# Kernel tuning notes

Hardware: AMD Instinct MI355X
Metric: run time of the kernel (lower is better)

Reference implementation:

```python
import jax, jax.numpy as jnp
import numpy as np

SLOPE = 25.0  # fast-sigmoid surrogate slope (snntorch default)

@jax.custom_vjp
def spike(u):
    # Heaviside spike with fast-sigmoid surrogate gradient
    return (u > 0).astype(u.dtype)

def _spike_fwd(u):
    return spike(u), u

def _spike_bwd(u, g):
    return (g / (1.0 + SLOPE * jnp.abs(u)) ** 2,)

spike.defvjp(_spike_fwd, _spike_bwd)


def setup_inputs() -> dict:
    key = jax.random.key(0)
    B, N_IN, T = 256, 700, 100
    H1, H2, O = 2048, 2048, 20
    ks = jax.random.split(key, 6)

    def lin(k, out_d, in_d):
        s = 1.0 / np.sqrt(in_d)
        kw, kb = jax.random.split(k)
        W = jax.random.uniform(kw, (out_d, in_d), minval=-s, maxval=s, dtype=jnp.float32)
        b = jax.random.uniform(kb, (out_d,), minval=-s, maxval=s, dtype=jnp.float32)
        return W, b

    W1, b1 = lin(ks[0], H1, N_IN)
    W2, b2 = lin(ks[1], H2, H1)
    V, _ = lin(ks[2], H2, H2)  # learned recurrent weight of RecurrentAhpc
    W3, b3 = lin(ks[3], O, H2)
    data = jax.random.normal(ks[4], (B, N_IN, T), dtype=jnp.float32)
    f32 = lambda v: jnp.asarray(v, jnp.float32)
    return dict(
        data=data,
        W1=W1, b1=b1, W2=W2, b2=b2, V=V, W3=W3, b3=b3,
        beta1=f32(0.9), thr1=f32(1.0),
        beta_r=f32(0.9), thr_r=f32(1.0),
        back_beta=f32(0.85), alpha=f32(0.6),
        beta2=f32(0.9), thr2=f32(1.0),
    )


def _forward(data, W1, b1, W2, b2, V, W3, b3,
             beta1, thr1, beta_r, thr_r, back_beta, alpha, beta2, thr2):
    B = data.shape[0]
    H1, H2, O = W1.shape[0], W2.shape[0], W3.shape[0]
    xs = jnp.transpose(data, (2, 0, 1))  # [T, B, N_in]
    z = lambda d: jnp.zeros((B, d), dtype=data.dtype)
    init = (z(H1), z(H2), z(H2), z(H2), z(O))  # mem1, mem_r, ahp, spk_r, mem2

    def step(carry, x_t):
        mem1, mem_r, ahp, spk_r, mem2 = carry
        # layer 1: Linear + Leaky (reset-by-subtract)
        mem1 = beta1 * mem1 + x_t @ W1.T + b1
        s1 = spike(mem1 - thr1)
        mem1 = mem1 - s1 * thr1
        # layer 2: Linear + recurrent AHP leaky neuron
        cur = s1 @ W2.T + b2 + spk_r @ V.T
        mem_r = beta_r * mem_r + cur - ahp
        s_r = spike(mem_r - thr_r)
        mem_r = mem_r - s_r * thr_r
        ahp = back_beta * ahp + alpha * s_r  # after-hyperpolarization current
        # layer 3: Linear + Leaky output
        mem2 = beta2 * mem2 + s_r @ W3.T + b3
        s2 = spike(mem2 - thr2)
        mem2 = mem2 - s2 * thr2
        return (mem1, mem_r, ahp, s_r, mem2), s2

    _, spk_rec = jax.lax.scan(step, init, xs)
    return spk_rec  # [T, B, num_outputs]


def reference(data, W1, b1, W2, b2, V, W3, b3,
              beta1, thr1, beta_r, thr_r, back_beta, alpha, beta2, thr2):
    return _forward(data, W1, b1, W2, b2, V, W3, b3,
                    beta1, thr1, beta_r, thr_r, back_beta, alpha, beta2, thr2)
```

## Files before the change

kernel.cpp:

```cpp
#include <hip/hip_runtime.h>
#include <hip/hip_bf16.h>
#include <cstdint>

#define T_STEPS 100
#define BATCH 256
#define NIN 700
#define H1 2048
#define H2 2048
#define NOUT 20
#define VKS 8
#define TCHUNK 10

typedef __attribute__((ext_vector_type(8))) short bf16x8;
typedef __attribute__((ext_vector_type(4))) float f32x4;
typedef unsigned long long ull;

__device__ __forceinline__ void async16(void* lds, const void* g) {
    __builtin_amdgcn_global_load_lds(
        (const __attribute__((address_space(1))) unsigned int*)g,
        (__attribute__((address_space(3))) unsigned int*)lds, 16, 0, 0);
}

__device__ __forceinline__ unsigned short f2bf(float x) {
    __hip_bfloat16 h = __float2bfloat16(x);
    return *(unsigned short*)&h;
}
__device__ __forceinline__ float bf2f(unsigned short u) {
    __hip_bfloat16 h = *(__hip_bfloat16*)&u;
    return __bfloat162float(h);
}

__device__ __forceinline__ void byte_to_u4(unsigned int byte, unsigned int* u) {
    #pragma unroll
    for (int p = 0; p < 4; ++p) {
        int bit = p << 1;
        u[p] = (((byte >> bit) & 1u) ? 0x3F80u : 0u)
             | (((byte >> (bit + 1)) & 1u) ? 0x3F800000u : 0u);
    }
}

__global__ __launch_bounds__(256) void split_kernel(
    const float* __restrict__ W2, const float* __restrict__ V,
    unsigned short* __restrict__ Bsplit)
{
    const size_t D = (size_t)2048 * 4096;
    size_t i = (size_t)blockIdx.x * 256 + threadIdx.x;
    int j = (int)(i >> 12), k = (int)(i & 4095);
    float w = (k < 2048) ? W2[(size_t)j * 2048 + k] : V[(size_t)j * 2048 + (k - 2048)];
    unsigned short h = f2bf(w);
    float r1 = w - bf2f(h);
    unsigned short m = f2bf(r1);
    float r2 = r1 - bf2f(m);
    unsigned short l = f2bf(r2);
    Bsplit[i] = h;
    Bsplit[D + i] = m;
    Bsplit[2 * D + i] = l;
}

__global__ __launch_bounds__(256) void w1split_kernel(
    const float* __restrict__ W1, unsigned short* __restrict__ W1f)
{
    const size_t P = (size_t)88 * 2048 * 8;
    int id = blockIdx.x * 256 + threadIdx.x;
    int g = id >> 11, j = id & 2047;
    unsigned short h8[8], m8[8], l8[8];
    #pragma unroll
    for (int e = 0; e < 8; ++e) {
        int k = g * 8 + e;
        float v = (k < NIN) ? W1[(size_t)j * NIN + k] : 0.f;
        unsigned short h = f2bf(v); float r1 = v - bf2f(h);
        unsigned short m = f2bf(r1); float r2 = r1 - bf2f(m);
        h8[e] = h; m8[e] = m; l8[e] = f2bf(r2);
    }
    size_t base = (((size_t)g * 2048) + j) * 8;
    *(uint4*)(W1f + base)         = *(uint4*)h8;
    *(uint4*)(W1f + P + base)     = *(uint4*)m8;
    *(uint4*)(W1f + 2 * P + base) = *(uint4*)l8;
}

__global__ __launch_bounds__(256) void l1m_kernel(
    const float* __restrict__ data, const unsigned short* __restrict__ W1f,
    const float* __restrict__ b1,
    const float* __restrict__ p_beta1, const float* __restrict__ p_thr1,
    ull* __restrict__ s1bits)
{
    __shared__ __align__(16) char smem[33280];
    unsigned short* Af = (unsigned short*)smem;
    const int tid = threadIdx.x, lane = tid & 63, w = tid >> 6;
    const int n16 = lane & 15, q = lane >> 4;
    const int jt = blockIdx.x & 7, b = blockIdx.x >> 3;
    const int j0w = jt * 256 + w * 64;
    const float* xb = data + (size_t)b * (NIN * T_STEPS);
    const size_t P = (size_t)88 * 2048 * 8;

    f32x4 acc[7][4] = {};
    for (int c = 0; c < 22; ++c) {
        const int kbase = c * 32;
        for (int it = tid; it < 448; it += 256) {
            int g = it / 112, t = it - g * 112;
            unsigned short h8[8], m8[8], l8[8];
            #pragma unroll
            for (int e = 0; e < 8; ++e) {
                int k = kbase + g * 8 + e;
                float v = (t < T_STEPS && k < NIN) ? xb[(size_t)k * T_STEPS + t] : 0.f;
                unsigned short h = f2bf(v); float r1 = v - bf2f(h);
                unsigned short m = f2bf(r1); float r2 = r1 - bf2f(m);
                h8[e] = h; m8[e] = m; l8[e] = f2bf(r2);
            }
            unsigned short* dst = Af + g * 896 + t * 8;
            *(uint4*)(dst)        = *(uint4*)h8;
            *(uint4*)(dst + 3584) = *(uint4*)m8;
            *(uint4*)(dst + 7168) = *(uint4*)l8;
        }
        __syncthreads();
        bf16x8 bh[4], bm[4], bl[4];
        const size_t gq = (size_t)(c * 4 + q);
        #pragma unroll
        for (int n = 0; n < 4; ++n) {
            size_t off = (gq * 2048 + (size_t)(j0w + n * 16 + n16)) * 8;
            bh[n] = *(const bf16x8*)(W1f + off);
            bm[n] = *(const bf16x8*)(W1f + P + off);
            bl[n] = *(const bf16x8*)(W1f + 2 * P + off);
        }
        #pragma unroll
        for (int m = 0; m < 7; ++m) {
            const unsigned short* ap = Af + q * 896 + (m * 16 + n16) * 8;
            bf16x8 ah = *(const bf16x8*)(ap);
            bf16x8 am = *(const bf16x8*)(ap + 3584);
            bf16x8 al = *(const bf16x8*)(ap + 7168);
            #pragma unroll
            for (int n = 0; n < 4; ++n) {
                acc[m][n] = __builtin_amdgcn_mfma_f32_16x16x32_bf16(ah, bh[n], acc[m][n], 0, 0, 0);
                acc[m][n] = __builtin_amdgcn_mfma_f32_16x16x32_bf16(ah, bm[n], acc[m][n], 0, 0, 0);
                acc[m][n] = __builtin_amdgcn_mfma_f32_16x16x32_bf16(am, bh[n], acc[m][n], 0, 0, 0);
                acc[m][n] = __builtin_amdgcn_mfma_f32_16x16x32_bf16(ah, bl[n], acc[m][n], 0, 0, 0);
                acc[m][n] = __builtin_amdgcn_mfma_f32_16x16x32_bf16(al, bh[n], acc[m][n], 0, 0, 0);
                acc[m][n] = __builtin_amdgcn_mfma_f32_16x16x32_bf16(am, bm[n], acc[m][n], 0, 0, 0);
            }
        }
        __syncthreads();
    }
    float* Cw = (float*)smem + w * (32 * 65);
    const float beta1 = *p_beta1, thr1 = *p_thr1;
    const float b1j = b1[j0w + lane];
    float mem = 0.f;
    for (int s = 0; s < 4; ++s) {
        #pragma unroll
        for (int mm = 0; mm < 2; ++mm) {
            int m = s * 2 + mm;
            if (m < 7) {
                #pragma unroll
                for (int n = 0; n < 4; ++n)
                    #pragma unroll
                    for (int r = 0; r < 4; ++r)
                        Cw[(mm * 16 + q * 4 + r) * 65 + n * 16 + n16] = acc[m][n][r];
            }
        }
        int tcnt = (s < 3) ? 32 : 4;
        for (int tt = 0; tt < tcnt; ++tt) {
            float v = Cw[tt * 65 + lane];
            mem = fmaf(beta1, mem, v) + b1j;
            bool pred = (mem - thr1) > 0.f;
            ull mask = __ballot(pred);
            if (pred) mem -= thr1;
            if (lane == 0) {
                int tg = s * 32 + tt;
                s1bits[((size_t)tg * BATCH + b) * 32 + jt * 4 + w] = mask;
            }
        }
    }
}

__global__ __launch_bounds__(256, 2) void xw2_kernel(
    const ull* __restrict__ bits0,
    const unsigned short* __restrict__ Bsplit,
    float* __restrict__ X2c)
{
    __shared__ __align__(16) unsigned short Alds[128 * 64];
    __shared__ __align__(16) unsigned short Blds[3 * 64 * 64];
    const int bid = blockIdx.x;
    const int x = bid & 7;
    const int i = bid >> 3;
    const int ntl = i / 20;
    const int mt = i - ntl * 20;
    const int n0 = (x * 4 + ntl) << 6;
    const int tid = threadIdx.x, lane = tid & 63, w = tid >> 6;
    const int ar = tid >> 1, ah2 = tid & 1;
    f32x4 acc[2][4] = {};
    for (int c = 0; c < 32; ++c) {
        const int kin = c << 6;
        {
            ull word = bits0[(size_t)(mt * 128 + ar) * 32 + c];
            unsigned int half = (unsigned int)(word >> (ah2 * 32));
            #pragma unroll
            for (int gi2 = 0; gi2 < 4; ++gi2) {
                int g = (ah2 << 2) + gi2;
                unsigned int u[4];
                byte_to_u4((half >> (gi2 * 8)) & 0xFFu, u);
                int slot = (ar << 3) + (g ^ (ar & 7));
                *(uint4*)(Alds + (slot << 3)) = *(uint4*)u;
            }
        }
        #pragma unroll
        for (int term = 0; term < 3; ++term) {
            const unsigned short* Bg = Bsplit + ((size_t)term << 23);
            #pragma unroll
            for (int ii = 0; ii < 2; ++ii) {
                int d = (w << 7) + (ii << 6) + lane;
                int row = d >> 3, g8 = d & 7;
                async16(Blds + (((term << 9) + (w << 7) + (ii << 6)) << 3),
                        Bg + (size_t)(n0 + row) * 4096 + kin + ((g8 ^ (row & 7)) << 3));
            }
        }
        __syncthreads();
        #pragma unroll
        for (int kk = 0; kk < 2; ++kk) {
            const int q = lane >> 4, k16 = (kk << 2) + q;
            bf16x8 af[2];
            #pragma unroll
            for (int ii = 0; ii < 2; ++ii) {
                int ra = (w << 5) + (ii << 4) + (lane & 15);
                af[ii] = *(const bf16x8*)(Alds + (((ra << 3) + (k16 ^ (ra & 7))) << 3));
            }
            #pragma unroll
            for (int term = 0; term < 3; ++term) {
                bf16x8 bfr[4];
                #pragma unroll
                for (int j = 0; j < 4; ++j) {
                    int rb = (j << 4) + (lane & 15);
                    bfr[j] = *(const bf16x8*)(Blds +
                              (((term << 9) + (rb << 3) + (k16 ^ (rb & 7))) << 3));
                }
                #pragma unroll
                for (int ii = 0; ii < 2; ++ii)
                    #pragma unroll
                    for (int j = 0; j < 4; ++j)
                        acc[ii][j] = __builtin_amdgcn_mfma_f32_16x16x32_bf16(
                            af[ii], bfr[j], acc[ii][j], 0, 0, 0);
            }
        }
        __syncthreads();
    }
    float* Xp = X2c + ((size_t)mt << 7) * 2048;
    #pragma unroll
    for (int ii = 0; ii < 2; ++ii) {
        int rg = (w << 5) + (ii << 4) + ((lane >> 4) << 2);
        #pragma unroll
        for (int j = 0; j < 4; ++j) {
            int cg = n0 + (j << 4) + (lane & 15);
            #pragma unroll
            for (int r = 0; r < 4; ++r)
                Xp[(size_t)(rg + r) * 2048 + cg] = acc[ii][j][r];
        }
    }
}

__global__ __launch_bounds__(256, 2) void vgemm_kernel(
    const ull* __restrict__ srb_in,
    const unsigned short* __restrict__ Bsplit,
    float* __restrict__ Cpart)
{
    __shared__ __align__(16) unsigned short Alds[256 * 64];
    __shared__ __align__(16) unsigned short Blds[3 * 64 * 64];
    const int bid = blockIdx.x;
    const int nt = bid & 31, ks = bid >> 5;
    const int n0 = nt << 6;
    const int tid = threadIdx.x, lane = tid & 63, w = tid >> 6;
    f32x4 acc[4][4] = {};
    for (int c = 0; c < 4; ++c) {
        const int kin = (ks << 8) + (c << 6);
        {
            ull word = srb_in[((size_t)tid << 5) + (ks << 2) + c];
            #pragma unroll
            for (int g8 = 0; g8 < 8; ++g8) {
                unsigned int u[4];
                byte_to_u4((unsigned int)(word >> (g8 << 3)) & 0xFFu, u);
                int gdst = (tid << 3) + (g8 ^ (tid & 7));
                *(uint4*)(Alds + (gdst << 3)) = *(uint4*)u;
            }
        }
        #pragma unroll
        for (int term = 0; term < 3; ++term) {
            const unsigned short* Bg = Bsplit + ((size_t)term << 23);
            #pragma unroll
            for (int ii = 0; ii < 2; ++ii) {
                int d = (w << 7) + (ii << 6) + lane;
                int row = d >> 3, g8 = d & 7;
                async16(Blds + (((term << 9) + (w << 7) + (ii << 6)) << 3),
                        Bg + (size_t)(n0 + row) * 4096 + 2048 + kin + ((g8 ^ (row & 7)) << 3));
            }
        }
        __syncthreads();
        #pragma unroll
        for (int kk = 0; kk < 2; ++kk) {
            const int q = lane >> 4, k16 = (kk << 2) + q;
            bf16x8 af[4];
            #pragma unroll
            for (int ii = 0; ii < 4; ++ii) {
                int ra = (w << 6) + (ii << 4) + (lane & 15);
                af[ii] = *(const bf16x8*)(Alds + (((ra << 3) + (k16 ^ (ra & 7))) << 3));
            }
            #pragma unroll
            for (int term = 0; term < 3; ++term) {
                bf16x8 bfr[4];
                #pragma unroll
                for (int j = 0; j < 4; ++j) {
                    int rb = (j << 4) + (lane & 15);
                    bfr[j] = *(const bf16x8*)(Blds +
                              (((term << 9) + (rb << 3) + (k16 ^ (rb & 7))) << 3));
                }
                #pragma unroll
                for (int ii = 0; ii < 4; ++ii)
                    #pragma unroll
                    for (int j = 0; j < 4; ++j)
                        acc[ii][j] = __builtin_amdgcn_mfma_f32_16x16x32_bf16(
                            af[ii], bfr[j], acc[ii][j], 0, 0, 0);
            }
        }
        __syncthreads();
    }
    float* Cp = Cpart + ((size_t)ks << 19);
    #pragma unroll
    for (int ii = 0; ii < 4; ++ii) {
        int rg = (w << 6) + (ii << 4) + ((lane >> 4) << 2);
        #pragma unroll
        for (int j = 0; j < 4; ++j) {
            int cg = n0 + (j << 4) + (lane & 15);
            #pragma unroll
            for (int r = 0; r < 4; ++r)
                Cp[(size_t)(rg + r) * 2048 + cg] = acc[ii][j][r];
        }
    }
}

__global__ __launch_bounds__(256) void l2fin_kernel(
    const float* __restrict__ Cpart, const float* __restrict__ X2t,
    const float* __restrict__ b2,
    float* __restrict__ mem_r, float* __restrict__ ahp,
    ull* __restrict__ srbits_out,
    const float* __restrict__ p_beta_r, const float* __restrict__ p_thr_r,
    const float* __restrict__ p_back_beta, const float* __restrict__ p_alpha)
{
    const int b = blockIdx.x, t = threadIdx.x;
    const int lane = t & 63, wv = t >> 6;
    const float beta_r = *p_beta_r, thr_r = *p_thr_r;
    const float bb = *p_back_beta, al = *p_alpha;
    #pragma unroll
    for (int u = 0; u < 8; ++u) {
        int j = t + (u << 8);
        size_t cidx = (size_t)b * 2048 + j;
        float x = 0.f;
        #pragma unroll
        for (int p = 0; p < VKS; ++p) x += Cpart[((size_t)p << 19) + cidx];
        float cur = x + X2t[cidx] + b2[j];
        float m = fmaf(beta_r, mem_r[cidx], cur) - ahp[cidx];
        bool pred = (m - thr_r) > 0.f;
        ull mask = __ballot(pred);
        float s = pred ? 1.f : 0.f;
        if (pred) m -= thr_r;
        mem_r[cidx] = m;
        ahp[cidx] = fmaf(bb, ahp[cidx], al * s);
        if (lane == 0) srbits_out[((size_t)b << 5) + (u << 2) + wv] = mask;
    }
}

__global__ __launch_bounds__(256) void w3out_kernel(
    const ull* __restrict__ srbits, const float* __restrict__ W3,
    const float* __restrict__ b3, float* __restrict__ out,
    const float* __restrict__ p_beta2, const float* __restrict__ p_thr2)
{
    __shared__ ull bitsLDS[T_STEPS * 32];
    __shared__ float red[4][10];
    const int b = blockIdx.x, tid = threadIdx.x, lane = tid & 63, wv = tid >> 6;
    for (int i = tid; i < T_STEPS * 32; i += 256)
        bitsLDS[i] = srbits[((size_t)(i >> 5) * BATCH + b) * 32 + (i & 31)];
    __syncthreads();
    const float beta2 = *p_beta2, thr2 = *p_thr2;
    for (int pass = 0; pass < 2; ++pass) {
        float w8[10][8];
        #pragma unroll
        for (int o = 0; o < 10; ++o) {
            const float4* wp = (const float4*)(W3 + (size_t)(pass * 10 + o) * 2048 + tid * 8);
            float4 a = wp[0], c = wp[1];
            w8[o][0] = a.x; w8[o][1] = a.y; w8[o][2] = a.z; w8[o][3] = a.w;
            w8[o][4] = c.x; w8[o][5] = c.y; w8[o][6] = c.z; w8[o][7] = c.w;
        }
        float m2 = 0.f;
        for (int t = 0; t < T_STEPS; ++t) {
            ull word = bitsLDS[(t << 5) + (tid >> 3)];
            unsigned int byte = (unsigned int)(word >> ((tid & 7) * 8)) & 0xFFu;
            float po[10];
            #pragma unroll
            for (int o = 0; o < 10; ++o) {
                float v = 0.f;
                #pragma unroll
                for (int e = 0; e < 8; ++e)
                    v += ((byte >> e) & 1u) ? w8[o][e] : 0.f;
                #pragma unroll
                for (int msk = 32; msk > 0; msk >>= 1)
                    v += __shfl_xor(v, msk, 64);
                po[o] = v;
            }
            if (lane == 0) {
                #pragma unroll
                for (int o = 0; o < 10; ++o) red[wv][o] = po[o];
            }
            __syncthreads();
            if (tid < 10) {
                float cur = red[0][tid] + red[1][tid] + red[2][tid] + red[3][tid]
                          + b3[pass * 10 + tid];
                float m = fmaf(beta2, m2, cur);
                bool pred = (m - thr2) > 0.f;
                float s2 = pred ? 1.f : 0.f;
                if (pred) m -= thr2;
                m2 = m;
                out[((size_t)t * BATCH + b) * NOUT + pass * 10 + tid] = s2;
            }
            __syncthreads();
        }
    }
}

extern "C" void kernel_launch(void* const* d_in, const int* in_sizes, int n_in,
                              void* d_out, int out_size, void* d_ws, size_t ws_size,
                              hipStream_t stream)
{
    const float* data   = (const float*)d_in[0];
    const float* W1     = (const float*)d_in[1];
    const float* b1     = (const float*)d_in[2];
    const float* W2     = (const float*)d_in[3];
    const float* b2     = (const float*)d_in[4];
    const float* V      = (const float*)d_in[5];
    const float* W3     = (const float*)d_in[6];
    const float* b3     = (const float*)d_in[7];
    const float* beta1  = (const float*)d_in[8];
    const float* thr1   = (const float*)d_in[9];
    const float* beta_r = (const float*)d_in[10];
    const float* thr_r  = (const float*)d_in[11];
    const float* back_beta = (const float*)d_in[12];
    const float* alpha  = (const float*)d_in[13];
    const float* beta2  = (const float*)d_in[14];
    const float* thr2   = (const float*)d_in[15];
    float* out = (float*)d_out;
    (void)in_sizes; (void)n_in; (void)out_size; (void)ws_size;

    const size_t PLANE = (size_t)BATCH * 32;

    char* p = (char*)d_ws;
    auto carve = [&](size_t bytes) {
        char* r = p; p += (bytes + 255) & ~(size_t)255; return r;
    };
    ull* s1bits = (ull*)carve((size_t)T_STEPS*BATCH*32*8);
    ull* srbAll = (ull*)carve((size_t)(T_STEPS+1)*BATCH*32*8);
    float* mem_r = (float*)carve((size_t)BATCH*H2*4);
    float* ahp   = (float*)carve((size_t)BATCH*H2*4);
    unsigned short* Bsplit = (unsigned short*)carve((size_t)3*2048*4096*2);
    float* Cpart = (float*)carve((size_t)VKS*BATCH*H2*4);
    float* X2c = (float*)carve((size_t)TCHUNK*BATCH*H2*4);
    unsigned short* W1f = (unsigned short*)carve((size_t)3*88*2048*8*2);

    hipMemsetAsync(srbAll, 0, PLANE*8, stream);
    hipMemsetAsync(mem_r, 0, (size_t)BATCH*H2*4, stream);
    hipMemsetAsync(ahp,  0, (size_t)BATCH*H2*4, stream);

    split_kernel<<<(2048*4096)/256, 256, 0, stream>>>(W2, V, Bsplit);
    w1split_kernel<<<704, 256, 0, stream>>>(W1, W1f);
    l1m_kernel<<<2048, 256, 0, stream>>>(data, W1f, b1, beta1, thr1, s1bits);

    for (int ck = 0; ck < T_STEPS / TCHUNK; ++ck) {
        const int t0 = ck * TCHUNK;
        xw2_kernel<<<640, 256, 0, stream>>>(s1bits + (size_t)t0*BATCH*32,
                                            Bsplit, X2c);
        for (int tt = 0; tt < TCHUNK; ++tt) {
            const int t = t0 + tt;
            vgemm_kernel<<<256, 256, 0, stream>>>(srbAll + (size_t)t*PLANE,
                                                  Bsplit, Cpart);
            l2fin_kernel<<<256, 256, 0, stream>>>(Cpart,
                                                  X2c + (size_t)tt*BATCH*H2, b2,
                                                  mem_r, ahp,
                                                  srbAll + (size_t)(t+1)*PLANE,
                                                  beta_r, thr_r, back_beta, alpha);
        }
    }
    w3out_kernel<<<256, 256, 0, stream>>>(srbAll + PLANE, W3, b3, out,
                                          beta2, thr2);
}
```

Baseline: 3.764 ms.

## Double-buffer LDS in recurrent GEMM and widen layer-2 finalize blocks

The recurrent V-GEMM kernel now preloads all four spike-bit words up front and double-buffers both the A and B LDS tiles. The next K chunk is staged while the current one feeds the MFMAs, which hides global-load latency behind compute. This roughly doubles LDS use and drops the two-blocks-per-CU launch bound. The layer-2 finalize kernel now uses 1024 threads per batch row instead of 256, with the ballot-word indexing adjusted, so each thread handles fewer elements per step.

```diff
diff --git a/kernel.cpp b/kernel.cpp
--- a/kernel.cpp
+++ b/kernel.cpp
@@ -255,30 +255,34 @@
     }
 }
 
-__global__ __launch_bounds__(256, 2) void vgemm_kernel(
+__global__ __launch_bounds__(256) void vgemm_kernel(
     const ull* __restrict__ srb_in,
     const unsigned short* __restrict__ Bsplit,
     float* __restrict__ Cpart)
 {
-    __shared__ __align__(16) unsigned short Alds[256 * 64];
-    __shared__ __align__(16) unsigned short Blds[3 * 64 * 64];
+    __shared__ __align__(16) unsigned short Alds[2][256 * 64];
+    __shared__ __align__(16) unsigned short Blds[2][3 * 64 * 64];
     const int bid = blockIdx.x;
     const int nt = bid & 31, ks = bid >> 5;
     const int n0 = nt << 6;
     const int tid = threadIdx.x, lane = tid & 63, w = tid >> 6;
-    f32x4 acc[4][4] = {};
-    for (int c = 0; c < 4; ++c) {
+    ull aw[4];
+    {
+        const ull* wp = srb_in + ((size_t)tid << 5) + (ks << 2);
+        aw[0] = wp[0]; aw[1] = wp[1]; aw[2] = wp[2]; aw[3] = wp[3];
+    }
+    auto stageA = [&](int c, int buf) {
+        ull word = aw[c];
+        #pragma unroll
+        for (int g8 = 0; g8 < 8; ++g8) {
+            unsigned int u[4];
+            byte_to_u4((unsigned int)(word >> (g8 << 3)) & 0xFFu, u);
+            int gdst = (tid << 3) + (g8 ^ (tid & 7));
+            *(uint4*)(Alds[buf] + (gdst << 3)) = *(uint4*)u;
+        }
+    };
+    auto stageB = [&](int c, int buf) {
         const int kin = (ks << 8) + (c << 6);
-        {
-            ull word = srb_in[((size_t)tid << 5) + (ks << 2) + c];
-            #pragma unroll
-            for (int g8 = 0; g8 < 8; ++g8) {
-                unsigned int u[4];
-                byte_to_u4((unsigned int)(word >> (g8 << 3)) & 0xFFu, u);
-                int gdst = (tid << 3) + (g8 ^ (tid & 7));
-                *(uint4*)(Alds + (gdst << 3)) = *(uint4*)u;
-            }
-        }
         #pragma unroll
         for (int term = 0; term < 3; ++term) {
             const unsigned short* Bg = Bsplit + ((size_t)term << 23);
@@ -286,11 +290,21 @@
             for (int ii = 0; ii < 2; ++ii) {
                 int d = (w << 7) + (ii << 6) + lane;
                 int row = d >> 3, g8 = d & 7;
-                async16(Blds + (((term << 9) + (w << 7) + (ii << 6)) << 3),
+                async16(Blds[buf] + (((term << 9) + (w << 7) + (ii << 6)) << 3),
                         Bg + (size_t)(n0 + row) * 4096 + 2048 + kin + ((g8 ^ (row & 7)) << 3));
             }
         }
-        __syncthreads();
+    };
+    f32x4 acc[4][4] = {};
+    stageB(0, 0);
+    stageA(0, 0);
+    __syncthreads();
+    for (int c = 0; c < 4; ++c) {
+        const int buf = c & 1;
+        if (c < 3) {
+            stageB(c + 1, buf ^ 1);
+            stageA(c + 1, buf ^ 1);
+        }
         #pragma unroll
         for (int kk = 0; kk < 2; ++kk) {
             const int q = lane >> 4, k16 = (kk << 2) + q;
@@ -298,7 +312,7 @@
             #pragma unroll
             for (int ii = 0; ii < 4; ++ii) {
                 int ra = (w << 6) + (ii << 4) + (lane & 15);
-                af[ii] = *(const bf16x8*)(Alds + (((ra << 3) + (k16 ^ (ra & 7))) << 3));
+                af[ii] = *(const bf16x8*)(Alds[buf] + (((ra << 3) + (k16 ^ (ra & 7))) << 3));
             }
             #pragma unroll
             for (int term = 0; term < 3; ++term) {
@@ -306,7 +320,7 @@
                 #pragma unroll
                 for (int j = 0; j < 4; ++j) {
                     int rb = (j << 4) + (lane & 15);
-                    bfr[j] = *(const bf16x8*)(Blds +
+                    bfr[j] = *(const bf16x8*)(Blds[buf] +
                               (((term << 9) + (rb << 3) + (k16 ^ (rb & 7))) << 3));
                 }
                 #pragma unroll
@@ -333,7 +347,7 @@
     }
 }
 
-__global__ __launch_bounds__(256) void l2fin_kernel(
+__global__ __launch_bounds__(1024) void l2fin_kernel(
     const float* __restrict__ Cpart, const float* __restrict__ X2t,
     const float* __restrict__ b2,
     float* __restrict__ mem_r, float* __restrict__ ahp,
@@ -341,14 +355,14 @@
     const float* __restrict__ p_beta_r, const float* __restrict__ p_thr_r,
     const float* __restrict__ p_back_beta, const float* __restrict__ p_alpha)
 {
-    const int b = blockIdx.x, t = threadIdx.x;
-    const int lane = t & 63, wv = t >> 6;
+    const int b = blockIdx.x, tid = threadIdx.x;
+    const int lane = tid & 63, wv = tid >> 6;
     const float beta_r = *p_beta_r, thr_r = *p_thr_r;
     const float bb = *p_back_beta, al = *p_alpha;
     #pragma unroll
-    for (int u = 0; u < 8; ++u) {
-        int j = t + (u << 8);
-        size_t cidx = (size_t)b * 2048 + j;
+    for (int u = 0; u < 2; ++u) {
+        int j = tid + (u << 10);
+        size_t cidx = ((size_t)b << 11) + j;
         float x = 0.f;
         #pragma unroll
         for (int p = 0; p < VKS; ++p) x += Cpart[((size_t)p << 19) + cidx];
@@ -360,7 +374,7 @@
         if (pred) m -= thr_r;
         mem_r[cidx] = m;
         ahp[cidx] = fmaf(bb, ahp[cidx], al * s);
-        if (lane == 0) srbits_out[((size_t)b << 5) + (u << 2) + wv] = mask;
+        if (lane == 0) srbits_out[((size_t)b << 5) + (u << 4) + wv] = mask;
     }
 }
 
@@ -475,11 +489,11 @@
             const int t = t0 + tt;
             vgemm_kernel<<<256, 256, 0, stream>>>(srbAll + (size_t)t*PLANE,
                                                   Bsplit, Cpart);
-            l2fin_kernel<<<256, 256, 0, stream>>>(Cpart,
-                                                  X2c + (size_t)tt*BATCH*H2, b2,
-                                                  mem_r, ahp,
-                                                  srbAll + (size_t)(t+1)*PLANE,
-                                                  beta_r, thr_r, back_beta, alpha);
+            l2fin_kernel<<<256, 1024, 0, stream>>>(Cpart,
+                                                   X2c + (size_t)tt*BATCH*H2, b2,
+                                                   mem_r, ahp,
+                                                   srbAll + (size_t)(t+1)*PLANE,
+                                                   beta_r, thr_r, back_beta, alpha);
         }
     }
     w3out_kernel<<<256, 256, 0, stream>>>(srbAll + PLANE, W3, b3, out,
```

Result: faster. 3.343 ms (-11.2%).
